# Kernel optimization log

Measured on AMD Instinct MI355X. Metric: run time of the kernel, lower is better.

## Reference

```python
import jax, jax.numpy as jnp
import numpy as np

NEG_SLOPE = 0.2  # PyG GATConv default


def _gcn_conv(x, src, dst, ew, W, b):
    # PyG GCNConv: add self-loops (weight 1), symmetric normalization, linear, scatter-add, bias.
    n = x.shape[0]
    loop = jnp.arange(n)
    src = jnp.concatenate([src, loop])
    dst = jnp.concatenate([dst, loop])
    ew = jnp.concatenate([ew, jnp.ones((n,), x.dtype)])
    deg = jax.ops.segment_sum(ew, dst, num_segments=n)
    dinv = jnp.where(deg > 0, 1.0 / jnp.sqrt(jnp.maximum(deg, 1e-12)), 0.0)
    norm = dinv[src] * ew * dinv[dst]          # [E']
    xw = x @ W.T                                # [n, out]
    out = jax.ops.segment_sum(norm[:, None] * xw[src], dst, num_segments=n)
    return out + b


def _gat_conv(x, src, dst, W, att_src, att_dst, b, concat_heads):
    # PyG GATConv: self-loops, per-head linear, additive attention with leaky_relu,
    # softmax over incoming edges per destination node, weighted scatter-add.
    n = x.shape[0]
    heads, ch = att_src.shape[1], att_src.shape[2]
    loop = jnp.arange(n)
    src = jnp.concatenate([src, loop])
    dst = jnp.concatenate([dst, loop])
    xw = (x @ W.T).reshape(n, heads, ch)        # [n, H, C]
    a_s = (xw * att_src).sum(-1)                 # [n, H]
    a_d = (xw * att_dst).sum(-1)                 # [n, H]
    e = jax.nn.leaky_relu(a_s[src] + a_d[dst], NEG_SLOPE)  # [E', H]
    emax = jax.ops.segment_max(e, dst, num_segments=n)      # self-loops guarantee non-empty segments
    p = jnp.exp(e - emax[dst])
    denom = jax.ops.segment_sum(p, dst, num_segments=n)
    alpha = p / (denom[dst] + 1e-16)
    out = jax.ops.segment_sum(alpha[..., None] * xw[src], dst, num_segments=n)  # [n, H, C]
    out = out.reshape(n, heads * ch) if concat_heads else out.mean(axis=1)
    return out + b


def setup_inputs() -> dict:
    key = jax.random.key(0)
    ks = jax.random.split(key, 20)
    T, N, E, EL = 16, 2048, 16384, 8192
    D_IN, HID, D_OUT = 64, 128, 64
    s = 0.05
    inp = {
        "x": jax.random.normal(ks[0], (T, N, D_IN), jnp.float32),
        "edge_index": jax.random.randint(ks[1], (T, 2, E), 0, N, dtype=jnp.int64),
        "edge_attr": jax.random.uniform(ks[2], (T, E), jnp.float32),
        "edge_label_index": jax.random.randint(ks[3], (2, EL), 0, T * N, dtype=jnp.int64),
        # GCNConv params (conv1: in->hid, conv2: hid->hid)
        "conv1_w": jax.random.normal(ks[4], (HID, D_IN), jnp.float32) * s,
        "conv1_b": jnp.zeros((HID,), jnp.float32),
        "conv2_w": jax.random.normal(ks[5], (HID, HID), jnp.float32) * s,
        "conv2_b": jnp.zeros((HID,), jnp.float32),
        # GATConv gat1: in -> hid, heads=4, concat
        "gat1_w": jax.random.normal(ks[6], (4 * HID, D_IN), jnp.float32) * s,
        "gat1_att_src": jax.random.normal(ks[7], (1, 4, HID), jnp.float32) * s,
        "gat1_att_dst": jax.random.normal(ks[8], (1, 4, HID), jnp.float32) * s,
        "gat1_b": jnp.zeros((4 * HID,), jnp.float32),
        # GATConv gat2: 4*hid -> out, heads=1, no concat
        "gat2_w": jax.random.normal(ks[9], (D_OUT, 4 * HID), jnp.float32) * s,
        "gat2_att_src": jax.random.normal(ks[10], (1, 1, D_OUT), jnp.float32) * s,
        "gat2_att_dst": jax.random.normal(ks[11], (1, 1, D_OUT), jnp.float32) * s,
        "gat2_b": jnp.zeros((D_OUT,), jnp.float32),
        # fc_hop: 2*hid -> num_nodes
        "fc_hop_w": jax.random.normal(ks[12], (N, 2 * HID), jnp.float32) * s,
        "fc_hop_b": jnp.zeros((N,), jnp.float32),
    }
    return inp


def reference(x, edge_index, edge_attr, edge_label_index,
              conv1_w, conv1_b, conv2_w, conv2_b,
              gat1_w, gat1_att_src, gat1_att_dst, gat1_b,
              gat2_w, gat2_att_src, gat2_att_dst, gat2_b,
              fc_hop_w, fc_hop_b):
    T, N, _ = x.shape

    # --- per-timestep hop-count branch (x_low and x_high are mathematically identical) ---
    def hop_step(x_t, ei_t, ew_t):
        h = jax.nn.relu(_gcn_conv(x_t, ei_t[0], ei_t[1], ew_t, conv1_w, conv1_b))
        h = jax.nn.relu(_gcn_conv(h, ei_t[0], ei_t[1], ew_t, conv2_w, conv2_b))
        comb = jnp.concatenate([h, h], axis=-1)   # [x_low, x_high] with identical branches
        return comb @ fc_hop_w.T + fc_hop_b       # [N, num_nodes]

    hop_out = jax.vmap(hop_step)(x, edge_index, edge_attr)  # [T, N, N]

    # --- link-prediction branch: GAT over time-flattened node set ---
    xf = x.reshape(T * N, x.shape[-1])
    ef = edge_index.transpose(1, 0, 2).reshape(2, -1)  # [2, T*E]; node ids stay < N (as in source)
    z = jax.nn.relu(_gat_conv(xf, ef[0], ef[1], gat1_w, gat1_att_src, gat1_att_dst, gat1_b, True))
    # dropout(p=0.5) is identity in eval mode
    z = _gat_conv(z, ef[0], ef[1], gat2_w, gat2_att_src, gat2_att_dst, gat2_b, False)
    link_pred = (z[edge_label_index[0]] * z[edge_label_index[1]]).sum(axis=-1)  # [EL]
    return link_pred, hop_out
```

## Files before the change

kernel.cpp:

```cpp
#include <hip/hip_runtime.h>
#include <stdint.h>

typedef __attribute__((ext_vector_type(8))) short short8;
typedef __attribute__((ext_vector_type(4))) float f32x4;

#define T_   16
#define N_   2048
#define E_   16384
#define NT   32768
#define EALL 262144
#define EL_  8192

static __device__ __forceinline__ short f2bf(float f){
  union { float f; uint32_t u; } v; v.f = f;
  uint32_t r = (v.u + 0x7FFFu + ((v.u >> 16) & 1u)) >> 16;
  return (short)r;
}
static __device__ __forceinline__ float lrelu(float x){ return x > 0.f ? x : 0.2f*x; }

__global__ void k_zero(int* __restrict__ p, int n){
  int i = blockIdx.x*256 + threadIdx.x;
  if(i < n) p[i] = 0;
}
__global__ void k_cnt(const int* __restrict__ ei, int* __restrict__ cnt){
  int id = blockIdx.x*256 + threadIdx.x;
  if(id >= EALL) return;
  int t = id >> 14, e = id & (E_-1);
  int d = ei[t*2*E_ + E_ + e];
  atomicAdd(&cnt[t*N_ + d], 1);
}
__global__ __launch_bounds__(1024) void k_scan(const int* __restrict__ cnt, int* __restrict__ off){
  __shared__ int part[1024];
  int tid = threadIdx.x;
  int base = tid*32;
  int loc[32]; int s = 0;
#pragma unroll
  for(int i=0;i<32;i++){ loc[i] = s; s += cnt[base+i]; }
  part[tid] = s; __syncthreads();
  for(int d=1; d<1024; d<<=1){
    int v = (tid>=d) ? part[tid-d] : 0;
    __syncthreads();
    part[tid] += v;
    __syncthreads();
  }
  int pre = (tid==0) ? 0 : part[tid-1];
#pragma unroll
  for(int i=0;i<32;i++) off[base+i] = pre + loc[i];
  if(tid == 1023) off[NT] = part[1023];
}
__global__ void k_copyi(const int* __restrict__ a, int* __restrict__ b, int n){
  int i = blockIdx.x*256 + threadIdx.x;
  if(i < n) b[i] = a[i];
}
__global__ void k_fill(const int* __restrict__ ei, int* __restrict__ cur, int* __restrict__ csr){
  int id = blockIdx.x*256 + threadIdx.x;
  if(id >= EALL) return;
  int t = id >> 14, e = id & (E_-1);
  int s = ei[t*2*E_ + e];
  int d = ei[t*2*E_ + E_ + e];
  int pos = atomicAdd(&cur[t*N_ + d], 1);
  csr[pos] = (id << 11) | s;
}

__global__ void k_degg(const float* __restrict__ ew, const int* __restrict__ off,
                       const int* __restrict__ csr, float* __restrict__ dinv){
  int n = blockIdx.x*256 + threadIdx.x;
  if(n >= NT) return;
  float s = 1.0f;
  for(int k=off[n]; k<off[n+1]; k++) s += ew[csr[k] >> 11];
  dinv[n] = rsqrtf(s);
}

__global__ void k_coef(const int* __restrict__ ei, const float* __restrict__ ew,
                       const float* __restrict__ dinv, float* __restrict__ coef){
  int id = blockIdx.x*256 + threadIdx.x;
  if(id >= EALL) return;
  int t = id >> 14, e = id & (E_-1);
  int s = ei[t*2*E_ + e];
  int d = ei[t*2*E_ + E_ + e];
  coef[id] = dinv[t*N_ + s] * ew[id] * dinv[t*N_ + d];
}

template<int TM,int TN,bool PREACT,bool EBIAS,bool ERELU,bool OBF16>
__global__ __launch_bounds__(256) void gemm_bt(
    const float* __restrict__ A, const float* __restrict__ ab,
    const float* __restrict__ B, const float* __restrict__ bias,
    float* __restrict__ Cf, short* __restrict__ Cb, int K, int N)
{
  const int lane = threadIdx.x & 63;
  const int wv   = threadIdx.x >> 6;
  const int wi = wv >> 1, wj = wv & 1;
  const int q = lane >> 4, r = lane & 15;
  const int m0 = blockIdx.y * (2*TM*16) + wi * (TM*16);
  const int n0 = blockIdx.x * (2*TN*16) + wj * (TN*16);

  f32x4 acc[TM][TN];
#pragma unroll
  for(int i=0;i<TM;i++)
#pragma unroll
    for(int j=0;j<TN;j++) acc[i][j] = (f32x4){0.f,0.f,0.f,0.f};

  for(int k0=0;k0<K;k0+=32){
    const int ka = k0 + q*8;
    short8 af[TM], bfr[TN];
#pragma unroll
    for(int i=0;i<TM;i++){
      const float* p = A + (size_t)(m0 + i*16 + r)*K + ka;
      float4 u0 = *(const float4*)p;
      float4 u1 = *(const float4*)(p+4);
      float vv[8] = {u0.x,u0.y,u0.z,u0.w,u1.x,u1.y,u1.z,u1.w};
      if (PREACT){
        const float* bb = ab + ka;
        float4 b0 = *(const float4*)bb;
        float4 b1 = *(const float4*)(bb+4);
        float bv[8] = {b0.x,b0.y,b0.z,b0.w,b1.x,b1.y,b1.z,b1.w};
#pragma unroll
        for(int u=0;u<8;u++) vv[u] = fmaxf(vv[u]+bv[u], 0.f);
      }
      short8 s;
#pragma unroll
      for(int u=0;u<8;u++) s[u] = f2bf(vv[u]);
      af[i] = s;
    }
#pragma unroll
    for(int j=0;j<TN;j++){
      const float* p = B + (size_t)(n0 + j*16 + r)*K + ka;
      float4 u0 = *(const float4*)p;
      float4 u1 = *(const float4*)(p+4);
      float vv[8] = {u0.x,u0.y,u0.z,u0.w,u1.x,u1.y,u1.z,u1.w};
      short8 s;
#pragma unroll
      for(int u=0;u<8;u++) s[u] = f2bf(vv[u]);
      bfr[j] = s;
    }
#pragma unroll
    for(int i=0;i<TM;i++)
#pragma unroll
      for(int j=0;j<TN;j++)
        acc[i][j] = __builtin_amdgcn_mfma_f32_16x16x32_bf16(af[i], bfr[j], acc[i][j], 0,0,0);
  }

#pragma unroll
  for(int i=0;i<TM;i++){
#pragma unroll
    for(int j=0;j<TN;j++){
#pragma unroll
      for(int rr=0;rr<4;rr++){
        int row = m0 + i*16 + q*4 + rr;
        int col = n0 + j*16 + r;
        float v = acc[i][j][rr];
        if(EBIAS) v += bias[col];
        if(ERELU) v = fmaxf(v, 0.f);
        if(OBF16) Cb[(size_t)row*N + col] = f2bf(v);
        else      Cf[(size_t)row*N + col] = v;
      }
    }
  }
}

__global__ __launch_bounds__(256) void hop_gemm(
    const short* __restrict__ Abf, const short* __restrict__ Bbf,
    const float* __restrict__ bias, float* __restrict__ out)
{
  const int lane = threadIdx.x & 63;
  const int wv   = threadIdx.x >> 6;
  const int wi = wv >> 1, wj = wv & 1;
  const int q = lane >> 4, r = lane & 15;
  const int t  = blockIdx.z;
  const int m0 = blockIdx.y * 128 + wi * 64;
  const int n0 = blockIdx.x * 128 + wj * 64;
  const short* Ab = Abf + (size_t)t * N_ * 128;

  f32x4 acc[4][4];
#pragma unroll
  for(int i=0;i<4;i++)
#pragma unroll
    for(int j=0;j<4;j++) acc[i][j] = (f32x4){0.f,0.f,0.f,0.f};

#pragma unroll
  for(int k0=0;k0<128;k0+=32){
    const int ka = k0 + q*8;
    short8 af[4], bfr[4];
#pragma unroll
    for(int i=0;i<4;i++) af[i]  = *(const short8*)(Ab  + (size_t)(m0 + i*16 + r)*128 + ka);
#pragma unroll
    for(int j=0;j<4;j++) bfr[j] = *(const short8*)(Bbf + (size_t)(n0 + j*16 + r)*128 + ka);
#pragma unroll
    for(int i=0;i<4;i++)
#pragma unroll
      for(int j=0;j<4;j++)
        acc[i][j] = __builtin_amdgcn_mfma_f32_16x16x32_bf16(af[i], bfr[j], acc[i][j], 0,0,0);
  }

#pragma unroll
  for(int i=0;i<4;i++){
#pragma unroll
    for(int j=0;j<4;j++){
#pragma unroll
      for(int rr=0;rr<4;rr++){
        int row = m0 + i*16 + q*4 + rr;
        int col = n0 + j*16 + r;
        out[((size_t)t*N_ + row)*N_ + col] = acc[i][j][rr] + bias[col];
      }
    }
  }
}

__global__ __launch_bounds__(256) void k_prep1(const float* __restrict__ xw1,
    const float* __restrict__ atts, const float* __restrict__ attd,
    float* __restrict__ x1s, float* __restrict__ as1, float* __restrict__ ad1){
  int d = blockIdx.x;
  int tid = threadIdx.x;
  int h = tid >> 6, lane = tid & 63;
  float2 v = *(const float2*)(xw1 + (size_t)d*512 + tid*2);
  *(float2*)(x1s + (size_t)d*512 + tid*2) = v;
  int c = lane*2;
  float2 a = *(const float2*)(atts + h*128 + c);
  float2 b = *(const float2*)(attd + h*128 + c);
  float s  = v.x*a.x + v.y*a.y;
  float dd = v.x*b.x + v.y*b.y;
  for(int o=32;o;o>>=1){ s += __shfl_down(s,o); dd += __shfl_down(dd,o); }
  if(lane == 0){ as1[d*4+h] = s; ad1[d*4+h] = dd; }
}

__global__ __launch_bounds__(1024) void k_den1(
    const int* __restrict__ off, const int* __restrict__ csr,
    const float* __restrict__ as1, const float* __restrict__ ad1,
    float* __restrict__ p1s, float* __restrict__ den1){
  int d = blockIdx.x;
  int t = threadIdx.x >> 6;
  int lane = threadIdx.x & 63;
  __shared__ float sden[16][4];
  float ad[4];
#pragma unroll
  for(int h=0;h<4;h++) ad[h] = ad1[d*4+h];
  float sum[4] = {0.f,0.f,0.f,0.f};
  int key = t*N_ + d;
  int beg = off[key], end = off[key+1];
  for(int k=beg+lane; k<end; k+=64){
    int s = csr[k] & (N_-1);
#pragma unroll
    for(int h=0;h<4;h++){
      float p = expf(lrelu(as1[s*4+h] + ad[h]));
      p1s[(size_t)k*4+h] = p;
      sum[h] += p;
    }
  }
#pragma unroll
  for(int h=0;h<4;h++)
    for(int o=32;o;o>>=1) sum[h] += __shfl_down(sum[h], o);
  if(lane == 0){
#pragma unroll
    for(int h=0;h<4;h++) sden[t][h] = sum[h];
  }
  __syncthreads();
  if(threadIdx.x < 4){
    int h = threadIdx.x;
    float s = 0.f;
#pragma unroll
    for(int w=0;w<16;w++) s += sden[w][h];
    den1[d*4+h] = s + expf(lrelu(as1[d*4+h] + ad[h]));
  }
}

__global__ __launch_bounds__(1024) void k_z1g(
    const int* __restrict__ off, const int* __restrict__ csr,
    const float* __restrict__ p1s, const float* __restrict__ den1,
    const float* __restrict__ as1, const float* __restrict__ ad1,
    const float* __restrict__ x1s, float* __restrict__ xw1){
  int d = blockIdx.x;
  int grp = threadIdx.x >> 7;
  int cid = threadIdx.x & 127;
  int h = cid >> 5;
  __shared__ f32x4 red[7][128];
  f32x4 acc = (f32x4){0.f,0.f,0.f,0.f};
  for(int t=grp; t<16; t+=8){
    int key = t*N_ + d;
    int beg = off[key], end = off[key+1];
    for(int k=beg; k<end; k++){
      int s = csr[k] & (N_-1);
      float p = p1s[(size_t)k*4 + h];
      f32x4 u = *(const f32x4*)(x1s + (size_t)s*512 + cid*4);
      acc += u * p;
    }
  }
  if(grp) red[grp-1][cid] = acc;
  __syncthreads();
  if(grp == 0){
#pragma unroll
    for(int g=0; g<7; g++) acc += red[g][cid];
    float deninv = 1.f/(den1[d*4+h] + 1e-16f);
    float pself = expf(lrelu(as1[d*4+h] + ad1[d*4+h]));
    f32x4 v = *(const f32x4*)(x1s + (size_t)d*512 + cid*4);
    f32x4 o = (acc + v*pself) * deninv;
    *(f32x4*)(xw1 + (size_t)d*512 + cid*4) = o;
  }
}

__global__ __launch_bounds__(256) void k_prep2(const float* __restrict__ xw2b,
    const float* __restrict__ atts, const float* __restrict__ attd,
    const float* __restrict__ b2,
    float* __restrict__ x2s, float* __restrict__ as2, float* __restrict__ ad2){
  int d = blockIdx.x*4 + (threadIdx.x >> 6);
  int lane = threadIdx.x & 63;
  float v = xw2b[(size_t)d*64 + lane];
  x2s[(size_t)d*64 + lane] = v;
  float vb = v - b2[lane];
  float s = vb*atts[lane], dd = vb*attd[lane];
  for(int o=32;o;o>>=1){ s += __shfl_down(s,o); dd += __shfl_down(dd,o); }
  if(lane == 0){ as2[d] = s; ad2[d] = dd; }
}

__global__ __launch_bounds__(1024) void k_den2(
    const int* __restrict__ off, const int* __restrict__ csr,
    const float* __restrict__ as2, const float* __restrict__ ad2,
    float* __restrict__ p2s, float* __restrict__ den2){
  int d = blockIdx.x;
  int t = threadIdx.x >> 6;
  int lane = threadIdx.x & 63;
  __shared__ float sden[16];
  float ad = ad2[d];
  float sum = 0.f;
  int key = t*N_ + d;
  int beg = off[key], end = off[key+1];
  for(int k=beg+lane; k<end; k+=64){
    int s = csr[k] & (N_-1);
    float p = expf(lrelu(as2[s] + ad));
    p2s[k] = p;
    sum += p;
  }
  for(int o=32;o;o>>=1) sum += __shfl_down(sum, o);
  if(lane == 0) sden[t] = sum;
  __syncthreads();
  if(threadIdx.x == 0){
    float s = 0.f;
#pragma unroll
    for(int w=0;w<16;w++) s += sden[w];
    den2[d] = s + expf(lrelu(as2[d] + ad));
  }
}

__global__ __launch_bounds__(1024) void k_z2g(
    const int* __restrict__ off, const int* __restrict__ csr,
    const float* __restrict__ p2s, const float* __restrict__ den2,
    const float* __restrict__ as2, const float* __restrict__ ad2,
    const float* __restrict__ x2s, float* __restrict__ xw2b){
  int d = blockIdx.x;
  int t = threadIdx.x >> 6;
  int lane = threadIdx.x & 63;
  __shared__ float red[16][64];
  float acc = 0.f;
  int key = t*N_ + d;
  int beg = off[key], end = off[key+1];
  for(int k=beg; k<end; k++){
    int s = csr[k] & (N_-1);
    acc += p2s[k] * x2s[(size_t)s*64 + lane];
  }
  red[t][lane] = acc;
  __syncthreads();
  if(t == 0){
    float tot = 0.f;
#pragma unroll
    for(int w=0;w<16;w++) tot += red[w][lane];
    float deninv = 1.f/(den2[d] + 1e-16f);
    float pself = expf(lrelu(as2[d] + ad2[d]));
    xw2b[(size_t)d*64 + lane] = (tot + pself*x2s[(size_t)d*64 + lane]) * deninv;
  }
}

__global__ void k_linkpred(const float* __restrict__ z2, const int* __restrict__ eli,
                           float* __restrict__ out){
  int pair = blockIdx.x*4 + (threadIdx.x >> 6);
  int lane = threadIdx.x & 63;
  if(pair >= EL_) return;
  int a = eli[pair], b = eli[EL_ + pair];
  float v = z2[(size_t)a*64 + lane] * z2[(size_t)b*64 + lane];
  for(int off=32; off; off >>= 1) v += __shfl_down(v, off);
  if(lane == 0) out[pair] = v;
}

template<int F>
__global__ __launch_bounds__(F) void k_gcng(
    const float* __restrict__ coef, const float* __restrict__ dinv,
    const float* __restrict__ feats, const int* __restrict__ off,
    const int* __restrict__ csr, float* __restrict__ out){
  int node = blockIdx.x;
  int ch = threadIdx.x;
  int t = node >> 11;
  float di = dinv[node];
  float acc = di*di*feats[(size_t)node*F + ch];
  int beg = off[node], end = off[node+1];
  for(int k=beg; k<end; k++){
    int v = csr[k];
    int eid = v >> 11;
    int gs = (t << 11) | (v & (N_-1));
    acc += coef[eid]*feats[(size_t)gs*F + ch];
  }
  out[(size_t)node*F + ch] = acc;
}

__global__ void k_fcsum(const float* __restrict__ fcw, short* __restrict__ wbf){
  int id = blockIdx.x*256 + threadIdx.x;
  if(id >= N_*128) return;
  int j = id >> 7, k = id & 127;
  wbf[id] = f2bf(fcw[j*256 + k] + fcw[j*256 + 128 + k]);
}

extern "C" void kernel_launch(void* const* d_in, const int* in_sizes, int n_in,
                              void* d_out, int out_size, void* d_ws, size_t ws_size,
                              hipStream_t stream) {
  const float* x       = (const float*)d_in[0];
  const int*   ei      = (const int*)d_in[1];
  const float* eattr   = (const float*)d_in[2];
  const int*   eli     = (const int*)d_in[3];
  const float* conv1_w = (const float*)d_in[4];
  const float* conv1_b = (const float*)d_in[5];
  const float* conv2_w = (const float*)d_in[6];
  const float* conv2_b = (const float*)d_in[7];
  const float* gat1_w  = (const float*)d_in[8];
  const float* g1as    = (const float*)d_in[9];
  const float* g1ad    = (const float*)d_in[10];
  const float* gat1_b  = (const float*)d_in[11];
  const float* gat2_w  = (const float*)d_in[12];
  const float* g2as    = (const float*)d_in[13];
  const float* g2ad    = (const float*)d_in[14];
  const float* gat2_b  = (const float*)d_in[15];
  const float* fcw     = (const float*)d_in[16];
  const float* fcb     = (const float*)d_in[17];

  char* wp = (char*)d_ws;
  auto alloc = [&](size_t bytes)->void*{ void* r = wp; wp += (bytes + 255) & ~(size_t)255; return r; };
  int*   cnt   = (int*)alloc((size_t)NT*4);
  int*   off   = (int*)alloc((size_t)(NT+1)*4);
  int*   cur   = (int*)alloc((size_t)NT*4);
  int*   csr   = (int*)alloc((size_t)EALL*4);
  float* as1   = (float*)alloc((size_t)N_*4*4);
  float* ad1   = (float*)alloc((size_t)N_*4*4);
  float* den1  = (float*)alloc((size_t)N_*4*4);
  float* p1s   = (float*)alloc((size_t)EALL*4*4);
  float* x1s   = (float*)alloc((size_t)N_*512*4);
  float* xw2b  = (float*)alloc((size_t)NT*64*4);
  float* as2   = (float*)alloc((size_t)N_*4);
  float* ad2   = (float*)alloc((size_t)N_*4);
  float* den2  = (float*)alloc((size_t)N_*4);
  float* p2s   = (float*)alloc((size_t)EALL*4);
  float* x2s   = (float*)alloc((size_t)N_*64*4);
  float* dinv  = (float*)alloc((size_t)NT*4);
  float* coef  = (float*)alloc((size_t)EALL*4);
  float* accx  = (float*)alloc((size_t)NT*64*4);
  float* h1    = (float*)alloc((size_t)NT*128*4);
  float* acch  = (float*)alloc((size_t)NT*128*4);
  short* h2bf  = (short*)alloc((size_t)NT*128*2);
  short* fcsbf = (short*)alloc((size_t)N_*128*2);

  float* outf     = (float*)d_out;
  float* link_out = outf;
  float* hop_out  = outf + EL_;
  float* xw1      = hop_out;

  dim3 blk(256);

  k_zero<<<dim3(NT/256), blk, 0, stream>>>(cnt, NT);
  k_cnt<<<dim3(EALL/256), blk, 0, stream>>>(ei, cnt);
  k_scan<<<dim3(1), dim3(1024), 0, stream>>>(cnt, off);
  k_copyi<<<dim3(NT/256), blk, 0, stream>>>(off, cur, NT);
  k_fill<<<dim3(EALL/256), blk, 0, stream>>>(ei, cur, csr);
  k_degg<<<dim3(NT/256), blk, 0, stream>>>(eattr, off, csr, dinv);

  gemm_bt<4,4,false,false,false,false><<<dim3(4,256), blk, 0, stream>>>(
      x, nullptr, gat1_w, nullptr, xw1, nullptr, 64, 512);
  k_prep1<<<dim3(N_), blk, 0, stream>>>(xw1, g1as, g1ad, x1s, as1, ad1);
  k_den1<<<dim3(N_), dim3(1024), 0, stream>>>(off, csr, as1, ad1, p1s, den1);
  k_z1g<<<dim3(N_), dim3(1024), 0, stream>>>(off, csr, p1s, den1, as1, ad1, x1s, xw1);
  gemm_bt<4,2,true,true,false,false><<<dim3(1,256), blk, 0, stream>>>(
      xw1, gat1_b, gat2_w, gat2_b, xw2b, nullptr, 512, 64);
  k_prep2<<<dim3(N_/4), blk, 0, stream>>>(xw2b, g2as, g2ad, gat2_b, x2s, as2, ad2);
  k_den2<<<dim3(N_), dim3(1024), 0, stream>>>(off, csr, as2, ad2, p2s, den2);
  k_z2g<<<dim3(N_), dim3(1024), 0, stream>>>(off, csr, p2s, den2, as2, ad2, x2s, xw2b);
  k_linkpred<<<dim3(EL_/4), blk, 0, stream>>>(xw2b, eli, link_out);

  k_coef<<<dim3(EALL/256), blk, 0, stream>>>(ei, eattr, dinv, coef);
  k_gcng<64><<<dim3(NT), dim3(64), 0, stream>>>(coef, dinv, x, off, csr, accx);
  gemm_bt<4,4,false,true,true,false><<<dim3(1,256), blk, 0, stream>>>(
      accx, nullptr, conv1_w, conv1_b, h1, nullptr, 64, 128);
  k_gcng<128><<<dim3(NT), dim3(128), 0, stream>>>(coef, dinv, h1, off, csr, acch);
  gemm_bt<4,4,false,true,true,true><<<dim3(1,256), blk, 0, stream>>>(
      acch, nullptr, conv2_w, conv2_b, nullptr, h2bf, 128, 128);
  k_fcsum<<<dim3((N_*128)/256), blk, 0, stream>>>(fcw, fcsbf);
  hop_gemm<<<dim3(16,16,16), blk, 0, stream>>>(h2bf, fcsbf, fcb, hop_out);
}
```

Before: 654.6 us.

## Merge small setup kernels, prefetch CSR indices, and halve GEMM row tiles

Folds the count-zeroing and fc-weight bf16 summation into one init kernel, and has the scan write the cursor array directly, removing two launches. The gather loops in the degree, GAT and GCN aggregation kernels now load the next CSR entry one iteration ahead to hide index-load latency. GEMM row tiles shrink from 4 to 2 with twice as many blocks for more parallelism. The coefficient kernel moves earlier in the sequence.

```diff
diff --git a/kernel.cpp b/kernel.cpp
--- a/kernel.cpp
+++ b/kernel.cpp
@@ -18,10 +18,18 @@
 }
 static __device__ __forceinline__ float lrelu(float x){ return x > 0.f ? x : 0.2f*x; }
 
-__global__ void k_zero(int* __restrict__ p, int n){
-  int i = blockIdx.x*256 + threadIdx.x;
-  if(i < n) p[i] = 0;
-}
+__global__ void k_init(const float* __restrict__ fcw, short* __restrict__ wbf,
+                       int* __restrict__ cnt){
+  int b = blockIdx.x;
+  if(b < 128){
+    cnt[b*256 + threadIdx.x] = 0;
+  } else {
+    int id = (b-128)*256 + threadIdx.x;
+    int j = id >> 7, k = id & 127;
+    wbf[id] = f2bf(fcw[j*256 + k] + fcw[j*256 + 128 + k]);
+  }
+}
+
 __global__ void k_cnt(const int* __restrict__ ei, int* __restrict__ cnt){
   int id = blockIdx.x*256 + threadIdx.x;
   if(id >= EALL) return;
@@ -29,7 +37,8 @@
   int d = ei[t*2*E_ + E_ + e];
   atomicAdd(&cnt[t*N_ + d], 1);
 }
-__global__ __launch_bounds__(1024) void k_scan(const int* __restrict__ cnt, int* __restrict__ off){
+__global__ __launch_bounds__(1024) void k_scan(const int* __restrict__ cnt,
+                                               int* __restrict__ off, int* __restrict__ cur){
   __shared__ int part[1024];
   int tid = threadIdx.x;
   int base = tid*32;
@@ -45,12 +54,8 @@
   }
   int pre = (tid==0) ? 0 : part[tid-1];
 #pragma unroll
-  for(int i=0;i<32;i++) off[base+i] = pre + loc[i];
+  for(int i=0;i<32;i++){ int v = pre + loc[i]; off[base+i] = v; cur[base+i] = v; }
   if(tid == 1023) off[NT] = part[1023];
-}
-__global__ void k_copyi(const int* __restrict__ a, int* __restrict__ b, int n){
-  int i = blockIdx.x*256 + threadIdx.x;
-  if(i < n) b[i] = a[i];
 }
 __global__ void k_fill(const int* __restrict__ ei, int* __restrict__ cur, int* __restrict__ csr){
   int id = blockIdx.x*256 + threadIdx.x;
@@ -66,8 +71,16 @@
                        const int* __restrict__ csr, float* __restrict__ dinv){
   int n = blockIdx.x*256 + threadIdx.x;
   if(n >= NT) return;
+  int beg = off[n], end = off[n+1];
   float s = 1.0f;
-  for(int k=off[n]; k<off[n+1]; k++) s += ew[csr[k] >> 11];
+  if(beg < end){
+    int v = csr[beg];
+    for(int k=beg; k<end; k++){
+      int vn = (k+1<end) ? csr[k+1] : 0;
+      s += ew[v >> 11];
+      v = vn;
+    }
+  }
   dinv[n] = rsqrtf(s);
 }
 
@@ -277,11 +290,15 @@
   for(int t=grp; t<16; t+=8){
     int key = t*N_ + d;
     int beg = off[key], end = off[key+1];
+    if(beg >= end) continue;
+    int v = csr[beg];
     for(int k=beg; k<end; k++){
-      int s = csr[k] & (N_-1);
+      int vn = (k+1<end) ? csr[k+1] : 0;
+      int s = v & (N_-1);
       float p = p1s[(size_t)k*4 + h];
       f32x4 u = *(const f32x4*)(x1s + (size_t)s*512 + cid*4);
       acc += u * p;
+      v = vn;
     }
   }
   if(grp) red[grp-1][cid] = acc;
@@ -352,9 +369,14 @@
   float acc = 0.f;
   int key = t*N_ + d;
   int beg = off[key], end = off[key+1];
-  for(int k=beg; k<end; k++){
-    int s = csr[k] & (N_-1);
-    acc += p2s[k] * x2s[(size_t)s*64 + lane];
+  if(beg < end){
+    int v = csr[beg];
+    for(int k=beg; k<end; k++){
+      int vn = (k+1<end) ? csr[k+1] : 0;
+      int s = v & (N_-1);
+      acc += p2s[k] * x2s[(size_t)s*64 + lane];
+      v = vn;
+    }
   }
   red[t][lane] = acc;
   __syncthreads();
@@ -390,20 +412,17 @@
   float di = dinv[node];
   float acc = di*di*feats[(size_t)node*F + ch];
   int beg = off[node], end = off[node+1];
-  for(int k=beg; k<end; k++){
-    int v = csr[k];
-    int eid = v >> 11;
-    int gs = (t << 11) | (v & (N_-1));
-    acc += coef[eid]*feats[(size_t)gs*F + ch];
+  if(beg < end){
+    int v = csr[beg];
+    for(int k=beg; k<end; k++){
+      int vn = (k+1<end) ? csr[k+1] : 0;
+      int eid = v >> 11;
+      int gs = (t << 11) | (v & (N_-1));
+      acc += coef[eid]*feats[(size_t)gs*F + ch];
+      v = vn;
+    }
   }
   out[(size_t)node*F + ch] = acc;
-}
-
-__global__ void k_fcsum(const float* __restrict__ fcw, short* __restrict__ wbf){
-  int id = blockIdx.x*256 + threadIdx.x;
-  if(id >= N_*128) return;
-  int j = id >> 7, k = id & 127;
-  wbf[id] = f2bf(fcw[j*256 + k] + fcw[j*256 + 128 + k]);
 }
 
 extern "C" void kernel_launch(void* const* d_in, const int* in_sizes, int n_in,
@@ -460,32 +479,30 @@
 
   dim3 blk(256);
 
-  k_zero<<<dim3(NT/256), blk, 0, stream>>>(cnt, NT);
+  k_init<<<dim3(128+1024), blk, 0, stream>>>(fcw, fcsbf, cnt);
   k_cnt<<<dim3(EALL/256), blk, 0, stream>>>(ei, cnt);
-  k_scan<<<dim3(1), dim3(1024), 0, stream>>>(cnt, off);
-  k_copyi<<<dim3(NT/256), blk, 0, stream>>>(off, cur, NT);
+  k_scan<<<dim3(1), dim3(1024), 0, stream>>>(cnt, off, cur);
   k_fill<<<dim3(EALL/256), blk, 0, stream>>>(ei, cur, csr);
   k_degg<<<dim3(NT/256), blk, 0, stream>>>(eattr, off, csr, dinv);
-
-  gemm_bt<4,4,false,false,false,false><<<dim3(4,256), blk, 0, stream>>>(
+  k_coef<<<dim3(EALL/256), blk, 0, stream>>>(ei, eattr, dinv, coef);
+
+  gemm_bt<2,4,false,false,false,false><<<dim3(4,512), blk, 0, stream>>>(
       x, nullptr, gat1_w, nullptr, xw1, nullptr, 64, 512);
   k_prep1<<<dim3(N_), blk, 0, stream>>>(xw1, g1as, g1ad, x1s, as1, ad1);
   k_den1<<<dim3(N_), dim3(1024), 0, stream>>>(off, csr, as1, ad1, p1s, den1);
   k_z1g<<<dim3(N_), dim3(1024), 0, stream>>>(off, csr, p1s, den1, as1, ad1, x1s, xw1);
-  gemm_bt<4,2,true,true,false,false><<<dim3(1,256), blk, 0, stream>>>(
+  gemm_bt<2,2,true,true,false,false><<<dim3(1,512), blk, 0, stream>>>(
       xw1, gat1_b, gat2_w, gat2_b, xw2b, nullptr, 512, 64);
   k_prep2<<<dim3(N_/4), blk, 0, stream>>>(xw2b, g2as, g2ad, gat2_b, x2s, as2, ad2);
   k_den2<<<dim3(N_), dim3(1024), 0, stream>>>(off, csr, as2, ad2, p2s, den2);
   k_z2g<<<dim3(N_), dim3(1024), 0, stream>>>(off, csr, p2s, den2, as2, ad2, x2s, xw2b);
   k_linkpred<<<dim3(EL_/4), blk, 0, stream>>>(xw2b, eli, link_out);
 
-  k_coef<<<dim3(EALL/256), blk, 0, stream>>>(ei, eattr, dinv, coef);
   k_gcng<64><<<dim3(NT), dim3(64), 0, stream>>>(coef, dinv, x, off, csr, accx);
-  gemm_bt<4,4,false,true,true,false><<<dim3(1,256), blk, 0, stream>>>(
+  gemm_bt<2,4,false,true,true,false><<<dim3(1,512), blk, 0, stream>>>(
       accx, nullptr, conv1_w, conv1_b, h1, nullptr, 64, 128);
   k_gcng<128><<<dim3(NT), dim3(128), 0, stream>>>(coef, dinv, h1, off, csr, acch);
-  gemm_bt<4,4,false,true,true,true><<<dim3(1,256), blk, 0, stream>>>(
+  gemm_bt<2,4,false,true,true,true><<<dim3(1,512), blk, 0, stream>>>(
       acch, nullptr, conv2_w, conv2_b, nullptr, h2bf, 128, 128);
-  k_fcsum<<<dim3((N_*128)/256), blk, 0, stream>>>(fcw, fcsbf);
   hop_gemm<<<dim3(16,16,16), blk, 0, stream>>>(h2bf, fcsbf, fcb, hop_out);
 }
```

Measured after the change: 682.2 us. 4.2% more time.
